# Kernel tuning notes

Hardware: AMD Instinct MI355X
Metric: run time of the kernel (lower is better)

The kernel has to match this reference:

```python
import jax, jax.numpy as jnp
import numpy as np

N_NODES = 50000


def _build_graph(edge_index):
    # Add self-loops (PyG GCNConv default) and compute symmetric normalization.
    n = N_NODES
    loops = jnp.arange(n, dtype=edge_index.dtype)
    src = jnp.concatenate([edge_index[0], loops])
    dst = jnp.concatenate([edge_index[1], loops])
    deg = jax.ops.segment_sum(jnp.ones_like(dst, dtype=jnp.float32), dst, num_segments=n)
    dinv = jax.lax.rsqrt(jnp.maximum(deg, 1e-12))
    norm = dinv[src] * dinv[dst]  # [E+N]
    return src, dst, norm


def _gcn_layer(h, src, dst, norm, W, b):
    # transform-then-propagate: out[dst] += norm * (h @ W)[src]
    h = h @ W  # [N, D_out]
    msg = h[src] * norm[:, None]  # [E+N, D_out]
    agg = jax.ops.segment_sum(msg, dst, num_segments=N_NODES)
    return agg + b


def setup_inputs() -> dict:
    key = jax.random.key(0)
    ks = jax.random.split(key, 8)
    in_dim, hid, out = 128, 64, 32
    n_edges = 800000
    x = jax.random.normal(ks[0], (N_NODES, in_dim), dtype=jnp.float32)
    edge_index = jax.random.randint(ks[1], (2, n_edges), 0, N_NODES, dtype=jnp.int32)
    W1 = jax.random.normal(ks[2], (in_dim, hid), dtype=jnp.float32) / np.sqrt(in_dim)
    b1 = jnp.zeros((hid,), jnp.float32)
    W2 = jax.random.normal(ks[3], (hid, out), dtype=jnp.float32) / np.sqrt(hid)
    b2 = jnp.zeros((out,), jnp.float32)
    attn_w = jax.random.normal(ks[4], (out, 1), dtype=jnp.float32) / np.sqrt(out)
    attn_b = jnp.zeros((1,), jnp.float32)
    return {"x": x, "edge_index": edge_index, "W1": W1, "b1": b1,
            "W2": W2, "b2": b2, "attn_w": attn_w, "attn_b": attn_b}


def reference(x, edge_index, W1, b1, W2, b2, attn_w, attn_b):
    src, dst, norm = _build_graph(edge_index)
    h = jax.nn.relu(_gcn_layer(x, src, dst, norm, W1, b1))
    h = jax.nn.relu(_gcn_layer(h, src, dst, norm, W2, b2))
    attn = jax.nn.sigmoid(h @ attn_w + attn_b)  # [N, 1]
    return h * attn
```

## Files before the change

### kernel.cpp

```cpp
#include <hip/hip_runtime.h>
#include <hip/hip_fp16.h>
#include <math.h>

#define N_NODES 50000
#define SLICE_SZ 6250

__device__ __forceinline__ void fma4(float4& a, float w, const float4& v) {
    a.x += w * v.x; a.y += w * v.y; a.z += w * v.z; a.w += w * v.w;
}

struct h2x2 { __half2 a, b; };

__global__ void count_kernel(const int* __restrict__ dst, int E,
                             int* __restrict__ counts, int* __restrict__ rank) {
    int i = blockIdx.x * blockDim.x + threadIdx.x;
    if (i < E) rank[i] = atomicAdd(&counts[dst[i]], 1);
}

__global__ void scan_block_kernel(const int* __restrict__ in, int n,
                                  int* __restrict__ outEx, int* __restrict__ blocksum) {
    __shared__ int s[256];
    int t = threadIdx.x, i = blockIdx.x * 256 + t;
    int v = (i < n) ? in[i] : 0;
    s[t] = v;
    __syncthreads();
    for (int off = 1; off < 256; off <<= 1) {
        int x = (t >= off) ? s[t - off] : 0;
        __syncthreads();
        s[t] += x;
        __syncthreads();
    }
    if (i < n) outEx[i] = s[t] - v;
    if (t == 255 && blocksum) blocksum[blockIdx.x] = s[255];
}

__global__ void finalize_kernel(const int* __restrict__ counts, const int* __restrict__ blocksum,
                                int n, int E, int* __restrict__ row_ptr,
                                float* __restrict__ dinv) {
    int i = blockIdx.x * blockDim.x + threadIdx.x;
    if (i < n) {
        row_ptr[i] += blocksum[i >> 8];
        dinv[i] = rsqrtf((float)(counts[i] + 1));
        if (i == 0) row_ptr[n] = E;
    }
}

__global__ void fill2_kernel(const int* __restrict__ src, const int* __restrict__ dst,
                             const int* __restrict__ rank, int E,
                             const int* __restrict__ row_ptr, const float* __restrict__ dinv,
                             int2* __restrict__ edges) {
    const int slice = blockIdx.x & 7;
    const int chunk = blockIdx.x >> 3;
    const int CS = (((E + 255) >> 8) + 3) & ~3;
    const int lo = chunk * CS;
    const int hi = min(E, lo + CS);
    const int slo = slice * SLICE_SZ, shi = slo + SLICE_SZ;
    if (lo >= E) return;
    const int quad_end = lo + ((hi - lo) & ~3);
    for (int i = lo + threadIdx.x * 4; i + 3 < quad_end + 4 && i + 3 < hi + 4 && i < quad_end; i += 1024) {
        int4 d4 = *(const int4*)&dst[i];
        #pragma unroll
        for (int k = 0; k < 4; ++k) {
            int d = (&d4.x)[k];
            if (d >= slo && d < shi) {
                int s = src[i + k];
                int p = row_ptr[d] + rank[i + k];
                edges[p] = make_int2(s, __float_as_int(dinv[s] * dinv[d]));
            }
        }
    }
    for (int i = quad_end + threadIdx.x; i < hi; i += 256) {
        int d = dst[i];
        if (d >= slo && d < shi) {
            int s = src[i];
            int p = row_ptr[d] + rank[i];
            edges[p] = make_int2(s, __float_as_int(dinv[s] * dinv[d]));
        }
    }
}

template<int DIN, int DOUT, int BM, int KC, bool HOUT>
__global__ __launch_bounds__(256, 2) void gemm_kernel(const float* __restrict__ A,
                                                      const float* __restrict__ W,
                                                      void* __restrict__ Cv, int n) {
    constexpr int NCG = DOUT / 4;
    constexpr int NRG = BM / 4;
    static_assert(NCG * NRG == 256, "thread mapping");
    constexpr int KG = KC / 4;
    constexpr int RSTEP = 256 / KG;
    __shared__ __align__(16) float ws[DIN * DOUT];
    __shared__ __align__(16) float xs[KC][BM + 4];
    const int t = threadIdx.x;
    for (int i = 4 * t; i < DIN * DOUT; i += 1024)
        *(float4*)&ws[i] = *(const float4*)&W[i];
    const int rowbase = blockIdx.x * BM;
    const int r0 = (t / NCG) * 4;
    const int c0 = (t % NCG) * 4;
    const int lk = (t % KG) * 4;
    const int lr = t / KG;
    float acc[4][4] = {};
    for (int kc = 0; kc < DIN; kc += KC) {
        __syncthreads();
        #pragma unroll
        for (int r = lr; r < BM; r += RSTEP) {
            int row = rowbase + r;
            if (row >= n) row = n - 1;
            float4 v = *(const float4*)&A[(size_t)row * DIN + kc + lk];
            xs[lk + 0][r] = v.x; xs[lk + 1][r] = v.y;
            xs[lk + 2][r] = v.z; xs[lk + 3][r] = v.w;
        }
        __syncthreads();
        #pragma unroll 8
        for (int k = 0; k < KC; ++k) {
            float ar[4], wr[4];
            *(float4*)ar = *(const float4*)&xs[k][r0];
            *(float4*)wr = *(const float4*)&ws[(kc + k) * DOUT + c0];
            #pragma unroll
            for (int i = 0; i < 4; ++i)
                #pragma unroll
                for (int j = 0; j < 4; ++j)
                    acc[i][j] += ar[i] * wr[j];
        }
    }
    #pragma unroll
    for (int i = 0; i < 4; ++i) {
        int row = rowbase + r0 + i;
        if (row < n) {
            if constexpr (HOUT) {
                union { uint2 u; __half2 h[2]; } pk;
                pk.h[0] = __floats2half2_rn(acc[i][0], acc[i][1]);
                pk.h[1] = __floats2half2_rn(acc[i][2], acc[i][3]);
                *(uint2*)((__half*)Cv + (size_t)row * DOUT + c0) = pk.u;
            } else {
                float4 v = make_float4(acc[i][0], acc[i][1], acc[i][2], acc[i][3]);
                *(float4*)&((float*)Cv)[(size_t)row * DOUT + c0] = v;
            }
        }
    }
}

__global__ __launch_bounds__(256) void gather64_fuse_kernel(
        const __half* __restrict__ XWh, const int* __restrict__ row_ptr,
        const int2* __restrict__ edges, const float* __restrict__ dinv,
        const float* __restrict__ b1, const float* __restrict__ W2,
        float* __restrict__ out, int n) {
    __shared__ float ws2R[64 * 33];
    const int t = threadIdx.x;
    for (int i = t; i < 64 * 32; i += 256) {
        int f = i >> 5, j = i & 31;
        ws2R[f * 33 + (((j & 7) << 2) | (j >> 3))] = W2[i];
    }
    __syncthreads();
    const int lane = t & 63;
    const int wid = t >> 6;
    const int fg = lane & 15, way = lane >> 4;
    const h2x2* __restrict__ XW4 = (const h2x2*)XWh;
    for (int it = 0; it < 4; ++it) {
        const int node = blockIdx.x * 16 + wid * 4 + it;
        if (node >= n) break;
        const int start = row_ptr[node];
        const int deg = row_ptr[node + 1] - start;
        const int K = deg + 1;
        int2 rec;
        if (lane == 0) {
            float dv = dinv[node];
            rec = make_int2(node, __float_as_int(dv * dv));
        } else if (lane <= deg) {
            rec = edges[start + lane - 1];
        } else {
            rec = make_int2(node, 0);
        }
        float4 acc = make_float4(0.f, 0.f, 0.f, 0.f);
        const int KP = (min(K, 64) + 3) & ~3;
        int k = way;
        #define G64_STEP(kk)                                                   \
            { int sv = __shfl(rec.x, (kk), 64);                                \
              float wgt = __int_as_float(__shfl(rec.y, (kk), 64));             \
              h2x2 rr = XW4[(size_t)sv * 16 + fg];                             \
              float2 a0 = __half22float2(rr.a), b0 = __half22float2(rr.b);     \
              acc.x += wgt * a0.x; acc.y += wgt * a0.y;                        \
              acc.z += wgt * b0.x; acc.w += wgt * b0.y; }
        for (; k + 12 < KP; k += 16) {
            G64_STEP(k) G64_STEP(k + 4) G64_STEP(k + 8) G64_STEP(k + 12)
        }
        for (; k < KP; k += 4) G64_STEP(k)
        #undef G64_STEP
        for (int kk = 64 + way; kk < K; kk += 4) {
            int2 p = edges[start + kk - 1];
            float wgt = __int_as_float(p.y);
            h2x2 rr = XW4[(size_t)p.x * 16 + fg];
            float2 a0 = __half22float2(rr.a), b0 = __half22float2(rr.b);
            acc.x += wgt * a0.x; acc.y += wgt * a0.y;
            acc.z += wgt * b0.x; acc.w += wgt * b0.y;
        }
        #pragma unroll
        for (int m = 16; m <= 32; m <<= 1) {
            acc.x += __shfl_xor(acc.x, m, 64);
            acc.y += __shfl_xor(acc.y, m, 64);
            acc.z += __shfl_xor(acc.z, m, 64);
            acc.w += __shfl_xor(acc.w, m, 64);
        }
        float4 b = ((const float4*)b1)[fg];
        float4 h;
        h.x = fmaxf(acc.x + b.x, 0.f);
        h.y = fmaxf(acc.y + b.y, 0.f);
        h.z = fmaxf(acc.z + b.z, 0.f);
        h.w = fmaxf(acc.w + b.w, 0.f);
        const int rbase = fg * 132;
        float py[8];
        #pragma unroll
        for (int s = 0; s < 8; ++s) {
            int idx = rbase + 4 * s + way;
            py[s] = h.x * ws2R[idx]
                  + h.y * ws2R[idx + 33]
                  + h.z * ws2R[idx + 66]
                  + h.w * ws2R[idx + 99];
        }
        #pragma unroll
        for (int m = 1; m <= 8; m <<= 1) {
            #pragma unroll
            for (int s = 0; s < 8; ++s) py[s] += __shfl_xor(py[s], m, 64);
        }
        if (fg == 0) {
            float4* o = (float4*)&out[(size_t)node * 32 + way * 8];
            o[0] = make_float4(py[0], py[1], py[2], py[3]);
            o[1] = make_float4(py[4], py[5], py[6], py[7]);
        }
    }
}

__global__ __launch_bounds__(256) void gather32_final_kernel(
        const float* __restrict__ XW, const int* __restrict__ row_ptr,
        const int2* __restrict__ edges, const float* __restrict__ dinv,
        const float* __restrict__ b2, const float* __restrict__ aw,
        const float* __restrict__ ab, float* __restrict__ out, int n) {
    const int t = threadIdx.x;
    const int lane = t & 63;
    const int wid = t >> 6;
    const int fg = lane & 7, way = lane >> 3;
    const float4* __restrict__ XW4 = (const float4*)XW;
    for (int it = 0; it < 4; ++it) {
        const int node = blockIdx.x * 16 + wid * 4 + it;
        if (node >= n) break;
        const int start = row_ptr[node];
        const int deg = row_ptr[node + 1] - start;
        const int K = deg + 1;
        int2 rec;
        if (lane == 0) {
            float dv = dinv[node];
            rec = make_int2(node, __float_as_int(dv * dv));
        } else if (lane <= deg) {
            rec = edges[start + lane - 1];
        } else {
            rec = make_int2(node, 0);
        }
        float4 acc = make_float4(0.f, 0.f, 0.f, 0.f);
        const int KP = (min(K, 64) + 7) & ~7;
        int k = way;
        #define G32_STEP(kk)                                                   \
            { int sv = __shfl(rec.x, (kk), 64);                                \
              float wgt = __int_as_float(__shfl(rec.y, (kk), 64));             \
              float4 v = XW4[(size_t)sv * 8 + fg];                             \
              fma4(acc, wgt, v); }
        for (; k + 24 < KP; k += 32) {
            G32_STEP(k) G32_STEP(k + 8) G32_STEP(k + 16) G32_STEP(k + 24)
        }
        for (; k < KP; k += 8) G32_STEP(k)
        #undef G32_STEP
        for (int kk = 64 + way; kk < K; kk += 8) {
            int2 p = edges[start + kk - 1];
            fma4(acc, __int_as_float(p.y), XW4[(size_t)p.x * 8 + fg]);
        }
        #pragma unroll
        for (int m = 8; m <= 32; m <<= 1) {
            acc.x += __shfl_xor(acc.x, m, 64);
            acc.y += __shfl_xor(acc.y, m, 64);
            acc.z += __shfl_xor(acc.z, m, 64);
            acc.w += __shfl_xor(acc.w, m, 64);
        }
        float4 b = ((const float4*)b2)[fg];
        float4 h;
        h.x = fmaxf(acc.x + b.x, 0.f);
        h.y = fmaxf(acc.y + b.y, 0.f);
        h.z = fmaxf(acc.z + b.z, 0.f);
        h.w = fmaxf(acc.w + b.w, 0.f);
        float4 a4 = ((const float4*)aw)[fg];
        float sca = h.x * a4.x + h.y * a4.y + h.z * a4.z + h.w * a4.w;
        sca += __shfl_xor(sca, 1, 64);
        sca += __shfl_xor(sca, 2, 64);
        sca += __shfl_xor(sca, 4, 64);
        float attn = 1.f / (1.f + __expf(-(sca + ab[0])));
        if (way == 0) {
            float4 r = make_float4(h.x * attn, h.y * attn, h.z * attn, h.w * attn);
            ((float4*)&out[(size_t)node * 32])[fg] = r;
        }
    }
}

extern "C" void kernel_launch(void* const* d_in, const int* in_sizes, int n_in,
                              void* d_out, int out_size, void* d_ws, size_t ws_size,
                              hipStream_t stream) {
    const float* x  = (const float*)d_in[0];
    const int*   ei = (const int*)d_in[1];
    const float* W1 = (const float*)d_in[2];
    const float* b1 = (const float*)d_in[3];
    const float* W2 = (const float*)d_in[4];
    const float* b2 = (const float*)d_in[5];
    const float* aw = (const float*)d_in[6];
    const float* ab = (const float*)d_in[7];
    float* out = (float*)d_out;

    const int n = N_NODES;
    const int E = in_sizes[1] / 2;
    const int* src = ei;
    const int* dst = ei + E;

    char* w = (char*)d_ws;
    auto alloc = [&](size_t bytes) { char* p = w; w += (bytes + 255) & ~(size_t)255; return p; };
    int*    counts   = (int*)   alloc((size_t)n * 4);
    int*    row_ptr  = (int*)   alloc((size_t)(n + 1) * 4);
    int*    rank     = (int*)   alloc((size_t)E * 4);
    int*    blocksum = (int*)   alloc(1024);
    float*  dinv     = (float*) alloc((size_t)n * 4);
    int2*   edges    = (int2*)  alloc((size_t)E * 8);
    __half* bufAh    = (__half*)alloc((size_t)n * 64 * 2);
    float*  bufB     = (float*) alloc((size_t)n * 32 * 4);

    const int nb = (n + 255) / 256;

    hipMemsetAsync(counts, 0, (size_t)n * 4, stream);
    count_kernel<<<(E + 255) / 256, 256, 0, stream>>>(dst, E, counts, rank);
    scan_block_kernel<<<nb, 256, 0, stream>>>(counts, n, row_ptr, blocksum);
    scan_block_kernel<<<1, 256, 0, stream>>>(blocksum, nb, blocksum, nullptr);
    finalize_kernel<<<nb, 256, 0, stream>>>(counts, blocksum, n, E, row_ptr, dinv);
    fill2_kernel<<<256 * 8, 256, 0, stream>>>(src, dst, rank, E, row_ptr, dinv, edges);

    gemm_kernel<128, 64, 64, 32, true><<<(n + 63) / 64, 256, 0, stream>>>(x, W1, bufAh, n);
    gather64_fuse_kernel<<<(n + 15) / 16, 256, 0, stream>>>(
        bufAh, row_ptr, edges, dinv, b1, W2, bufB, n);
    gather32_final_kernel<<<(n + 15) / 16, 256, 0, stream>>>(
        bufB, row_ptr, edges, dinv, b2, aw, ab, out, n);
}
```

Baseline: 237.4 us.

## Split layer-1 gather into two feature-half passes and store layer-2 XW as fp16

The first GEMM now writes its fp16 output as two 32-column planes, one per feature half. Layer-1 aggregation runs as two gather passes, one per plane, so each pass touches a smaller working set that fits the cache better. The fused W2 projection is removed from the gather and replaced by a separate GEMM that reads a new fp32 h1 buffer and writes fp16 for the layer-2 gather, which halves that gather's read bytes. The cost is an extra kernel launch, a second pass over the edge list, and a 64-wide fp32 round trip for h1 through memory.

```diff
diff --git a/kernel.cpp b/kernel.cpp
--- a/kernel.cpp
+++ b/kernel.cpp
@@ -79,7 +79,7 @@
     }
 }
 
-template<int DIN, int DOUT, int BM, int KC, bool HOUT>
+template<int DIN, int DOUT, int BM, int KC, int OMODE>
 __global__ __launch_bounds__(256, 2) void gemm_kernel(const float* __restrict__ A,
                                                       const float* __restrict__ W,
                                                       void* __restrict__ Cv, int n) {
@@ -126,35 +126,35 @@
     for (int i = 0; i < 4; ++i) {
         int row = rowbase + r0 + i;
         if (row < n) {
-            if constexpr (HOUT) {
+            if constexpr (OMODE == 0) {
+                float4 v = make_float4(acc[i][0], acc[i][1], acc[i][2], acc[i][3]);
+                *(float4*)&((float*)Cv)[(size_t)row * DOUT + c0] = v;
+            } else {
                 union { uint2 u; __half2 h[2]; } pk;
                 pk.h[0] = __floats2half2_rn(acc[i][0], acc[i][1]);
                 pk.h[1] = __floats2half2_rn(acc[i][2], acc[i][3]);
-                *(uint2*)((__half*)Cv + (size_t)row * DOUT + c0) = pk.u;
-            } else {
-                float4 v = make_float4(acc[i][0], acc[i][1], acc[i][2], acc[i][3]);
-                *(float4*)&((float*)Cv)[(size_t)row * DOUT + c0] = v;
+                if constexpr (OMODE == 1) {
+                    const int hp = c0 >> 5, c = c0 & 31;
+                    *(uint2*)((__half*)Cv + (size_t)hp * ((size_t)n << 5)
+                              + (size_t)row * 32 + c) = pk.u;
+                } else {
+                    *(uint2*)((__half*)Cv + (size_t)row * DOUT + c0) = pk.u;
+                }
             }
         }
     }
 }
 
-__global__ __launch_bounds__(256) void gather64_fuse_kernel(
-        const __half* __restrict__ XWh, const int* __restrict__ row_ptr,
-        const int2* __restrict__ edges, const float* __restrict__ dinv,
-        const float* __restrict__ b1, const float* __restrict__ W2,
-        float* __restrict__ out, int n) {
-    __shared__ float ws2R[64 * 33];
+__global__ __launch_bounds__(256) void gather64_pass_kernel(
+        const __half* __restrict__ plane,
+        const int* __restrict__ row_ptr, const int2* __restrict__ edges,
+        const float* __restrict__ dinv, const float* __restrict__ b1h,
+        float* __restrict__ h1, int n, int half) {
     const int t = threadIdx.x;
-    for (int i = t; i < 64 * 32; i += 256) {
-        int f = i >> 5, j = i & 31;
-        ws2R[f * 33 + (((j & 7) << 2) | (j >> 3))] = W2[i];
-    }
-    __syncthreads();
     const int lane = t & 63;
     const int wid = t >> 6;
-    const int fg = lane & 15, way = lane >> 4;
-    const h2x2* __restrict__ XW4 = (const h2x2*)XWh;
+    const int fg = lane & 7, way = lane >> 3;
+    const h2x2* __restrict__ P = (const h2x2*)plane;
     for (int it = 0; it < 4; ++it) {
         const int node = blockIdx.x * 16 + wid * 4 + it;
         if (node >= n) break;
@@ -171,66 +171,47 @@
             rec = make_int2(node, 0);
         }
         float4 acc = make_float4(0.f, 0.f, 0.f, 0.f);
-        const int KP = (min(K, 64) + 3) & ~3;
+        const int KP = (min(K, 64) + 7) & ~7;
         int k = way;
-        #define G64_STEP(kk)                                                   \
+        #define GP_STEP(kk)                                                    \
             { int sv = __shfl(rec.x, (kk), 64);                                \
               float wgt = __int_as_float(__shfl(rec.y, (kk), 64));             \
-              h2x2 rr = XW4[(size_t)sv * 16 + fg];                             \
-              float2 a0 = __half22float2(rr.a), b0 = __half22float2(rr.b);     \
-              acc.x += wgt * a0.x; acc.y += wgt * a0.y;                        \
-              acc.z += wgt * b0.x; acc.w += wgt * b0.y; }
-        for (; k + 12 < KP; k += 16) {
-            G64_STEP(k) G64_STEP(k + 4) G64_STEP(k + 8) G64_STEP(k + 12)
-        }
-        for (; k < KP; k += 4) G64_STEP(k)
-        #undef G64_STEP
-        for (int kk = 64 + way; kk < K; kk += 4) {
+              h2x2 rr = P[(size_t)sv * 8 + fg];                                \
+              float2 f0 = __half22float2(rr.a), f1 = __half22float2(rr.b);     \
+              acc.x += wgt * f0.x; acc.y += wgt * f0.y;                        \
+              acc.z += wgt * f1.x; acc.w += wgt * f1.y; }
+        for (; k + 8 < KP; k += 16) { GP_STEP(k) GP_STEP(k + 8) }
+        for (; k < KP; k += 8) GP_STEP(k)
+        #undef GP_STEP
+        for (int kk = 64 + way; kk < K; kk += 8) {
             int2 p = edges[start + kk - 1];
             float wgt = __int_as_float(p.y);
-            h2x2 rr = XW4[(size_t)p.x * 16 + fg];
-            float2 a0 = __half22float2(rr.a), b0 = __half22float2(rr.b);
-            acc.x += wgt * a0.x; acc.y += wgt * a0.y;
-            acc.z += wgt * b0.x; acc.w += wgt * b0.y;
+            h2x2 rr = P[(size_t)p.x * 8 + fg];
+            float2 f0 = __half22float2(rr.a), f1 = __half22float2(rr.b);
+            acc.x += wgt * f0.x; acc.y += wgt * f0.y;
+            acc.z += wgt * f1.x; acc.w += wgt * f1.y;
         }
         #pragma unroll
-        for (int m = 16; m <= 32; m <<= 1) {
+        for (int m = 8; m <= 32; m <<= 1) {
             acc.x += __shfl_xor(acc.x, m, 64);
             acc.y += __shfl_xor(acc.y, m, 64);
             acc.z += __shfl_xor(acc.z, m, 64);
             acc.w += __shfl_xor(acc.w, m, 64);
         }
-        float4 b = ((const float4*)b1)[fg];
-        float4 h;
-        h.x = fmaxf(acc.x + b.x, 0.f);
-        h.y = fmaxf(acc.y + b.y, 0.f);
-        h.z = fmaxf(acc.z + b.z, 0.f);
-        h.w = fmaxf(acc.w + b.w, 0.f);
-        const int rbase = fg * 132;
-        float py[8];
-        #pragma unroll
-        for (int s = 0; s < 8; ++s) {
-            int idx = rbase + 4 * s + way;
-            py[s] = h.x * ws2R[idx]
-                  + h.y * ws2R[idx + 33]
-                  + h.z * ws2R[idx + 66]
-                  + h.w * ws2R[idx + 99];
-        }
-        #pragma unroll
-        for (int m = 1; m <= 8; m <<= 1) {
-            #pragma unroll
-            for (int s = 0; s < 8; ++s) py[s] += __shfl_xor(py[s], m, 64);
-        }
-        if (fg == 0) {
-            float4* o = (float4*)&out[(size_t)node * 32 + way * 8];
-            o[0] = make_float4(py[0], py[1], py[2], py[3]);
-            o[1] = make_float4(py[4], py[5], py[6], py[7]);
+        if (way == 0) {
+            float4 b = ((const float4*)b1h)[fg];
+            float4 h;
+            h.x = fmaxf(acc.x + b.x, 0.f);
+            h.y = fmaxf(acc.y + b.y, 0.f);
+            h.z = fmaxf(acc.z + b.z, 0.f);
+            h.w = fmaxf(acc.w + b.w, 0.f);
+            *(float4*)&h1[(size_t)node * 64 + half * 32 + 4 * fg] = h;
         }
     }
 }
 
 __global__ __launch_bounds__(256) void gather32_final_kernel(
-        const float* __restrict__ XW, const int* __restrict__ row_ptr,
+        const __half* __restrict__ XWh, const int* __restrict__ row_ptr,
         const int2* __restrict__ edges, const float* __restrict__ dinv,
         const float* __restrict__ b2, const float* __restrict__ aw,
         const float* __restrict__ ab, float* __restrict__ out, int n) {
@@ -238,7 +219,7 @@
     const int lane = t & 63;
     const int wid = t >> 6;
     const int fg = lane & 7, way = lane >> 3;
-    const float4* __restrict__ XW4 = (const float4*)XW;
+    const h2x2* __restrict__ P = (const h2x2*)XWh;
     for (int it = 0; it < 4; ++it) {
         const int node = blockIdx.x * 16 + wid * 4 + it;
         if (node >= n) break;
@@ -260,16 +241,20 @@
         #define G32_STEP(kk)                                                   \
             { int sv = __shfl(rec.x, (kk), 64);                                \
               float wgt = __int_as_float(__shfl(rec.y, (kk), 64));             \
-              float4 v = XW4[(size_t)sv * 8 + fg];                             \
-              fma4(acc, wgt, v); }
-        for (; k + 24 < KP; k += 32) {
-            G32_STEP(k) G32_STEP(k + 8) G32_STEP(k + 16) G32_STEP(k + 24)
-        }
+              h2x2 rr = P[(size_t)sv * 8 + fg];                                \
+              float2 f0 = __half22float2(rr.a), f1 = __half22float2(rr.b);     \
+              acc.x += wgt * f0.x; acc.y += wgt * f0.y;                        \
+              acc.z += wgt * f1.x; acc.w += wgt * f1.y; }
+        for (; k + 8 < KP; k += 16) { G32_STEP(k) G32_STEP(k + 8) }
         for (; k < KP; k += 8) G32_STEP(k)
         #undef G32_STEP
         for (int kk = 64 + way; kk < K; kk += 8) {
             int2 p = edges[start + kk - 1];
-            fma4(acc, __int_as_float(p.y), XW4[(size_t)p.x * 8 + fg]);
+            float wgt = __int_as_float(p.y);
+            h2x2 rr = P[(size_t)p.x * 8 + fg];
+            float2 f0 = __half22float2(rr.a), f1 = __half22float2(rr.b);
+            acc.x += wgt * f0.x; acc.y += wgt * f0.y;
+            acc.z += wgt * f1.x; acc.w += wgt * f1.y;
         }
         #pragma unroll
         for (int m = 8; m <= 32; m <<= 1) {
@@ -324,7 +309,8 @@
     float*  dinv     = (float*) alloc((size_t)n * 4);
     int2*   edges    = (int2*)  alloc((size_t)E * 8);
     __half* bufAh    = (__half*)alloc((size_t)n * 64 * 2);
-    float*  bufB     = (float*) alloc((size_t)n * 32 * 4);
+    float*  h1buf    = (float*) alloc((size_t)n * 64 * 4);
+    __half* bufCh    = (__half*)alloc((size_t)n * 32 * 2);
 
     const int nb = (n + 255) / 256;
 
@@ -335,9 +321,12 @@
     finalize_kernel<<<nb, 256, 0, stream>>>(counts, blocksum, n, E, row_ptr, dinv);
     fill2_kernel<<<256 * 8, 256, 0, stream>>>(src, dst, rank, E, row_ptr, dinv, edges);
 
-    gemm_kernel<128, 64, 64, 32, true><<<(n + 63) / 64, 256, 0, stream>>>(x, W1, bufAh, n);
-    gather64_fuse_kernel<<<(n + 15) / 16, 256, 0, stream>>>(
-        bufAh, row_ptr, edges, dinv, b1, W2, bufB, n);
+    gemm_kernel<128, 64, 64, 32, 1><<<(n + 63) / 64, 256, 0, stream>>>(x, W1, bufAh, n);
+    gather64_pass_kernel<<<(n + 15) / 16, 256, 0, stream>>>(
+        bufAh,                 row_ptr, edges, dinv, b1,      h1buf, n, 0);
+    gather64_pass_kernel<<<(n + 15) / 16, 256, 0, stream>>>(
+        bufAh + (size_t)n * 32, row_ptr, edges, dinv, b1 + 32, h1buf, n, 1);
+    gemm_kernel<64, 32, 128, 32, 2><<<(n + 127) / 128, 256, 0, stream>>>(h1buf, W2, bufCh, n);
     gather32_final_kernel<<<(n + 15) / 16, 256, 0, stream>>>(
-        bufB, row_ptr, edges, dinv, b2, aw, ab, out, n);
-}
+        bufCh, row_ptr, edges, dinv, b2, aw, ab, out, n);
+}
```

Result: no change. 239.1 us (+0.7%).
